# Optimization experiments

Measured on AMD Instinct MI355X. Metric: run time of the kernel, lower is better.

Reference implementation:

```python
import jax, jax.numpy as jnp
import numpy as np

B, CF, HH, WW = 32, 768, 28, 28
M, NH = 32, 1024
BETA = 0.05

def _lin(key, out_d, in_d):
    k1, k2 = jax.random.split(key)
    s = 1.0 / np.sqrt(in_d)
    W = jax.random.uniform(k1, (out_d, in_d), minval=-s, maxval=s, dtype=jnp.float32)
    b = jax.random.uniform(k2, (out_d,), minval=-s, maxval=s, dtype=jnp.float32)
    return W, b

def setup_inputs() -> dict:
    key = jax.random.key(0)
    ks = jax.random.split(key, 16)
    inp = {
        'F': jax.random.normal(ks[0], (B, CF, HH, WW), dtype=jnp.float32),
        'A': jax.random.uniform(ks[1], (B, M, HH, WW), dtype=jnp.float32),
        'C': jax.random.normal(ks[2], (1, M * CF), dtype=jnp.float32),
    }
    names = ['xi', 'hi', 'xf', 'hf', 'xo', 'ho', 'xc', 'hc']
    for i, n in enumerate(names):
        in_d = CF if n[0] == 'x' else NH
        W, b = _lin(ks[3 + i], NH, in_d)
        inp['W' + n] = W
        inp['b' + n] = b
    return inp

def reference(F, A, C, Wxi, bxi, Whi, bhi, Wxf, bxf, Whf, bhf, Wxo, bxo, Who, bho, Wxc, bxc, Whc, bhc):
    b = F.shape[0]
    hw = F.shape[2] * F.shape[3]
    m = A.shape[1]
    # BAP: avg-pool of F * A_i over spatial dims, for each attention map -> [B, M, Cf]
    V = jnp.einsum('bchw,bmhw->bmc', F, A) / hw
    V = V.reshape(b, -1)  # [B, M*Cf]
    # RCLoss (center update + detached MSE)
    tmp = jnp.sum(V - C, axis=0)  # [M*Cf]
    C_new = C + (BETA * tmp / b)[None, :]
    diff = jax.lax.stop_gradient(V) - jax.lax.stop_gradient(C_new)
    rcloss = jnp.mean(diff * diff)
    # LSTM over M steps (note: original uses sigmoid for all gates via Sig_i)
    X_seq = V.reshape(b, m, -1).transpose(1, 0, 2)  # [M, B, Cf]
    h0 = jnp.zeros((b, Whi.shape[0]), dtype=V.dtype)
    c0 = jnp.zeros((b, Whi.shape[0]), dtype=V.dtype)
    def step(carry, X):
        H, Cc = carry
        I = jax.nn.sigmoid(X @ Wxi.T + bxi + H @ Whi.T + bhi)
        Fg = jax.nn.sigmoid(X @ Wxf.T + bxf + H @ Whf.T + bhf)
        O = jax.nn.sigmoid(X @ Wxo.T + bxo + H @ Who.T + bho)
        Ct = jnp.tanh(X @ Wxc.T + bxc + H @ Whc.T + bhc)
        Cc = Fg * Cc + I * Ct
        H = O * jnp.tanh(Cc)
        return (H, Cc), None
    (H, _), _ = jax.lax.scan(step, (h0, c0), X_seq)
    return (H, rcloss, C_new)
```

## Files before the change

kernel.cpp:

```cpp
#include <hip/hip_runtime.h>
#include <math.h>

#define CF 768
#define MM 32
#define HW 784
#define MCF 24576
#define BETA 0.05f

typedef __attribute__((ext_vector_type(8))) short bf16x8;
typedef __attribute__((ext_vector_type(4))) float f32x4;

__device__ __forceinline__ float dot4(float4 a, float4 b, float acc) {
    acc = fmaf(a.x, b.x, acc); acc = fmaf(a.y, b.y, acc);
    acc = fmaf(a.z, b.z, acc); acc = fmaf(a.w, b.w, acc);
    return acc;
}

__device__ __forceinline__ unsigned short bf16rne(float x) {
    unsigned int bits = __float_as_uint(x);
    unsigned int r = (bits + 0x7fffu + ((bits >> 16) & 1u)) >> 16;
    return (unsigned short)r;
}
__device__ __forceinline__ float bf2f(unsigned short u) {
    return __uint_as_float(((unsigned int)u) << 16);
}
__device__ __forceinline__ float sigf(float x) { return 1.f / (1.f + __expf(-x)); }

#define KA_CT 96
#define KA_PAD 15

__global__ __launch_bounds__(256) void kA2(const float* __restrict__ F,
                                           const float* __restrict__ A,
                                           unsigned short* __restrict__ Vbf) {
    __shared__ float4 Fs[2][KA_CT][KA_PAD];
    __shared__ float4 As[2][32][KA_PAD];
    const int b = blockIdx.x >> 3;
    const int cbase = (blockIdx.x & 7) * KA_CT;
    const int t = threadIdx.x;
    const int tx = t & 31;
    const int ty = t >> 5;
    const int c0 = tx * 3, m0 = ty * 4;
    const float4* F4 = (const float4*)F;
    const float4* A4 = (const float4*)A;

    int i0 = t;          int fc0 = i0 / 14, fq0 = i0 - fc0 * 14;
    int i1 = t + 256;    int fc1 = i1 / 14, fq1 = i1 - fc1 * 14;
    int i2 = t + 512;    int fc2 = i2 / 14, fq2 = i2 - fc2 * 14;
    int i3 = t + 768;    int fc3 = i3 / 14, fq3 = i3 - fc3 * 14;
    int i4 = t + 1024;   int fc4 = i4 / 14, fq4 = i4 - fc4 * 14;
    int i5 = t + 1280;   int fc5 = (t < 64) ? (i5 / 14) : 0, fq5 = (t < 64) ? (i5 - (i5 / 14) * 14) : 0;
    int a0i = t;         int ac0 = a0i / 14, aq0 = a0i - ac0 * 14;
    int a1i = t + 256;   int ac1 = (t < 192) ? (a1i / 14) : 0, aq1 = (t < 192) ? (a1i - (a1i / 14) * 14) : 0;

    size_t fb0 = (size_t)(b * CF + cbase + fc0) * 196 + fq0;
    size_t fb1 = (size_t)(b * CF + cbase + fc1) * 196 + fq1;
    size_t fb2 = (size_t)(b * CF + cbase + fc2) * 196 + fq2;
    size_t fb3 = (size_t)(b * CF + cbase + fc3) * 196 + fq3;
    size_t fb4 = (size_t)(b * CF + cbase + fc4) * 196 + fq4;
    size_t fb5 = (size_t)(b * CF + cbase + fc5) * 196 + fq5;
    size_t ab0 = (size_t)(b * 32 + ac0) * 196 + aq0;
    size_t ab1 = (size_t)(b * 32 + ac1) * 196 + aq1;

    float4 fr0, fr1, fr2, fr3, fr4, fr5, ar0, ar1;
    float acc[4][3];
    #pragma unroll
    for (int i = 0; i < 4; ++i)
        #pragma unroll
        for (int j = 0; j < 3; ++j) acc[i][j] = 0.f;

    fr0 = F4[fb0]; fr1 = F4[fb1]; fr2 = F4[fb2]; fr3 = F4[fb3]; fr4 = F4[fb4];
    if (t < 64) fr5 = F4[fb5];
    ar0 = A4[ab0];
    if (t < 192) ar1 = A4[ab1];
    Fs[0][fc0][fq0] = fr0; Fs[0][fc1][fq1] = fr1; Fs[0][fc2][fq2] = fr2;
    Fs[0][fc3][fq3] = fr3; Fs[0][fc4][fq4] = fr4;
    if (t < 64) Fs[0][fc5][fq5] = fr5;
    As[0][ac0][aq0] = ar0;
    if (t < 192) As[0][ac1][aq1] = ar1;

    for (int ch = 0; ch < 14; ++ch) {
        int buf = ch & 1;
        __syncthreads();
        if (ch + 1 < 14) {
            size_t off = (size_t)(ch + 1) * 14;
            fr0 = F4[fb0 + off]; fr1 = F4[fb1 + off]; fr2 = F4[fb2 + off];
            fr3 = F4[fb3 + off]; fr4 = F4[fb4 + off];
            if (t < 64) fr5 = F4[fb5 + off];
            ar0 = A4[ab0 + off];
            if (t < 192) ar1 = A4[ab1 + off];
        }
        #pragma unroll 2
        for (int q = 0; q < 14; ++q) {
            float4 a_0 = As[buf][m0 + 0][q];
            float4 a_1 = As[buf][m0 + 1][q];
            float4 a_2 = As[buf][m0 + 2][q];
            float4 a_3 = As[buf][m0 + 3][q];
            float4 f_0 = Fs[buf][c0 + 0][q];
            float4 f_1 = Fs[buf][c0 + 1][q];
            float4 f_2 = Fs[buf][c0 + 2][q];
            acc[0][0] = dot4(a_0, f_0, acc[0][0]); acc[0][1] = dot4(a_0, f_1, acc[0][1]); acc[0][2] = dot4(a_0, f_2, acc[0][2]);
            acc[1][0] = dot4(a_1, f_0, acc[1][0]); acc[1][1] = dot4(a_1, f_1, acc[1][1]); acc[1][2] = dot4(a_1, f_2, acc[1][2]);
            acc[2][0] = dot4(a_2, f_0, acc[2][0]); acc[2][1] = dot4(a_2, f_1, acc[2][1]); acc[2][2] = dot4(a_2, f_2, acc[2][2]);
            acc[3][0] = dot4(a_3, f_0, acc[3][0]); acc[3][1] = dot4(a_3, f_1, acc[3][1]); acc[3][2] = dot4(a_3, f_2, acc[3][2]);
        }
        if (ch + 1 < 14) {
            int nb = buf ^ 1;
            Fs[nb][fc0][fq0] = fr0; Fs[nb][fc1][fq1] = fr1; Fs[nb][fc2][fq2] = fr2;
            Fs[nb][fc3][fq3] = fr3; Fs[nb][fc4][fq4] = fr4;
            if (t < 64) Fs[nb][fc5][fq5] = fr5;
            As[nb][ac0][aq0] = ar0;
            if (t < 192) As[nb][ac1][aq1] = ar1;
        }
    }
    #pragma unroll
    for (int i = 0; i < 4; ++i)
        #pragma unroll
        for (int j = 0; j < 3; ++j)
            Vbf[(size_t)(b * 32 + m0 + i) * 768 + cbase + c0 + j] =
                bf16rne(acc[i][j] * (1.f / 784.f));
}

__global__ __launch_bounds__(256) void kB1(const unsigned short* __restrict__ Vbf,
                                           const float* __restrict__ C,
                                           float* __restrict__ Cnew_out,
                                           float* __restrict__ partial) {
    int j = blockIdx.x * 256 + threadIdx.x;
    float c = C[j];
    float s = 0.f;
    for (int b = 0; b < 32; ++b) s += bf2f(Vbf[(size_t)b * MCF + j]);
    float cn = c + BETA * (s * (1.f / 32.f) - c);
    Cnew_out[j] = cn;
    float ds = 0.f;
    for (int b = 0; b < 32; ++b) {
        float d = bf2f(Vbf[(size_t)b * MCF + j]) - cn;
        ds = fmaf(d, d, ds);
    }
    __shared__ float red[256];
    red[threadIdx.x] = ds;
    __syncthreads();
    for (int off = 128; off > 0; off >>= 1) {
        if (threadIdx.x < off) red[threadIdx.x] += red[threadIdx.x + off];
        __syncthreads();
    }
    if (threadIdx.x == 0) partial[blockIdx.x] = red[0];
}

__global__ void kB2(const float* __restrict__ partial, float* __restrict__ out) {
    if (threadIdx.x == 0) {
        float s = 0.f;
        for (int i = 0; i < 96; ++i) s += partial[i];
        out[0] = s / (32.f * 24576.f);
    }
}

__global__ __launch_bounds__(256) void kPrepX(
    const float* __restrict__ Wxi, const float* __restrict__ Wxf,
    const float* __restrict__ Wxo, const float* __restrict__ Wxc,
    unsigned short* __restrict__ Wxbf) {
    int gid = blockIdx.x * 256 + threadIdx.x;
    int row = gid / 96;
    int kq = (gid - row * 96) * 8;
    int g = row >> 10, j = row & 1023;
    const float* Wg = (g == 0) ? Wxi : (g == 1) ? Wxf : (g == 2) ? Wxo : Wxc;
    const float* src = Wg + (size_t)j * CF + kq;
    float4 f0 = *(const float4*)src;
    float4 f1 = *(const float4*)(src + 4);
    unsigned short u[8];
    u[0] = bf16rne(f0.x); u[1] = bf16rne(f0.y); u[2] = bf16rne(f0.z); u[3] = bf16rne(f0.w);
    u[4] = bf16rne(f1.x); u[5] = bf16rne(f1.y); u[6] = bf16rne(f1.z); u[7] = bf16rne(f1.w);
    *(uint4*)&Wxbf[(size_t)row * CF + kq] = *(const uint4*)u;
}

__global__ __launch_bounds__(512) void kC3(
    const unsigned short* __restrict__ Vbf,
    const unsigned short* __restrict__ Wxbf,
    const float* __restrict__ bxi, const float* __restrict__ bxf,
    const float* __restrict__ bxo, const float* __restrict__ bxc,
    const float* __restrict__ bhi, const float* __restrict__ bhf,
    const float* __restrict__ bho, const float* __restrict__ bhc,
    unsigned short* __restrict__ Xbf) {
    __shared__ unsigned short Asg[512 * 8];
    const int bx = blockIdx.x;
    const int by = blockIdx.y;
    const int t = threadIdx.x;
    const int lane = t & 63;
    const int w = t >> 6;
    const int n = lane & 15;
    const int q = lane >> 4;
    const int mbase = bx * 64;

    const int st_row = (w & 3) * 16 + n;
    const int st_kb  = (w >> 2) * 4 + q;
    const int st_rg  = mbase + st_row;
    const int st_vrow = (st_rg & 31) * 32 + (st_rg >> 5);
    const unsigned short* st_src = Vbf + (size_t)st_vrow * CF + st_kb * 8;

    const int nb = by * 128 + w * 16;
    const unsigned short* Brow = Wxbf + (size_t)(nb + n) * CF + q * 8;

    f32x4 acc[4];
    #pragma unroll
    for (int g = 0; g < 4; ++g) acc[g] = (f32x4){0.f, 0.f, 0.f, 0.f};

    uint4 st = *(const uint4*)st_src;
    for (int kc = 0; kc < 12; ++kc) {
        __syncthreads();
        *(uint4*)&Asg[t * 8] = st;
        __syncthreads();
        if (kc + 1 < 12) st = *(const uint4*)(st_src + (kc + 1) * 64);
        #pragma unroll
        for (int p = 0; p < 2; ++p) {
            bf16x8 bfr = *(const bf16x8*)(Brow + kc * 64 + p * 32);
            #pragma unroll
            for (int g = 0; g < 4; ++g) {
                bf16x8 a = *(const bf16x8*)&Asg[((p * 4 + g) * 64 + lane) * 8];
                acc[g] = __builtin_amdgcn_mfma_f32_16x16x32_bf16(a, bfr, acc[g], 0, 0, 0);
            }
        }
    }

    const int gg = by >> 3;
    const int j = (by & 7) * 128 + w * 16 + n;
    const float* bx_ = (gg == 0) ? bxi : (gg == 1) ? bxf : (gg == 2) ? bxo : bxc;
    const float* bh_ = (gg == 0) ? bhi : (gg == 1) ? bhf : (gg == 2) ? bho : bhc;
    const float bias = bx_[j] + bh_[j];
    #pragma unroll
    for (int g = 0; g < 4; ++g) {
        #pragma unroll
        for (int rr = 0; rr < 4; ++rr) {
            int rg = mbase + g * 16 + q * 4 + rr;
            int tt = rg >> 5, bb = rg & 31;
            Xbf[((size_t)(tt * 4 + gg) * 32 + bb) * 1024 + j] = bf16rne(acc[g][rr] + bias);
        }
    }
}

__global__ __launch_bounds__(256) void kPrep(
    const float* __restrict__ Whi, const float* __restrict__ Whf,
    const float* __restrict__ Who, const float* __restrict__ Whc,
    unsigned short* __restrict__ Wbf) {
    size_t tid8 = ((size_t)blockIdx.x * 256 + threadIdx.x) * 8;
    int row = (int)(tid8 >> 10);
    int k = (int)(tid8 & 1023);
    int g = row >> 10, j = row & 1023;
    const float* Wg = (g == 0) ? Whi : (g == 1) ? Whf : (g == 2) ? Who : Whc;
    const float* src = Wg + (size_t)j * 1024 + k;
    float4 f0 = *(const float4*)src;
    float4 f1 = *(const float4*)(src + 4);
    unsigned short u[8];
    u[0] = bf16rne(f0.x); u[1] = bf16rne(f0.y); u[2] = bf16rne(f0.z); u[3] = bf16rne(f0.w);
    u[4] = bf16rne(f1.x); u[5] = bf16rne(f1.y); u[6] = bf16rne(f1.z); u[7] = bf16rne(f1.w);
    *(uint4*)&Wbf[tid8] = *(const uint4*)u;
}

__global__ __launch_bounds__(512) void kStep(
    const unsigned short* __restrict__ Wbf,
    const unsigned short* __restrict__ Xbf,
    const unsigned short* __restrict__ Hprev,
    unsigned short* __restrict__ Hnext,
    float* __restrict__ Cst,
    float* __restrict__ outH,
    int step) {
    __shared__ float pbuf[8][32][17];
    __shared__ float sbuf[32][17];
    const int bi = blockIdx.x;
    const int jbase = bi * 4;
    const int t = threadIdx.x;
    const int lane = t & 63;
    const int w = t >> 6;
    const int n = lane & 15;
    const int q = lane >> 4;

    if (step > 0) {
        const int g = n >> 2, jj = n & 3;
        const unsigned short* Wrow = Wbf + ((size_t)(g * 1024 + jbase + jj)) * 1024 + w * 128;
        const unsigned short* hb0 = Hprev + (size_t)n * 1024 + w * 128;
        const unsigned short* hb1 = Hprev + (size_t)(n + 16) * 1024 + w * 128;
        f32x4 acc0 = {0.f, 0.f, 0.f, 0.f};
        f32x4 acc1 = {0.f, 0.f, 0.f, 0.f};
        #pragma unroll
        for (int ks = 0; ks < 4; ++ks) {
            int k = ks * 32 + q * 8;
            bf16x8 bfrag = *(const bf16x8*)(Wrow + k);
            bf16x8 a0 = *(const bf16x8*)(hb0 + k);
            bf16x8 a1 = *(const bf16x8*)(hb1 + k);
            acc0 = __builtin_amdgcn_mfma_f32_16x16x32_bf16(a0, bfrag, acc0, 0, 0, 0);
            acc1 = __builtin_amdgcn_mfma_f32_16x16x32_bf16(a1, bfrag, acc1, 0, 0, 0);
        }
        #pragma unroll
        for (int r = 0; r < 4; ++r) {
            pbuf[w][q * 4 + r][n] = acc0[r];
            pbuf[w][16 + q * 4 + r][n] = acc1[r];
        }
    }
    __syncthreads();
    {
        int b = t >> 4, nn = t & 15;
        int g = nn >> 2, jj = nn & 3;
        float s = bf2f(Xbf[(((size_t)step * 4 + g) * 32 + b) * 1024 + jbase + jj]);
        if (step > 0) {
            #pragma unroll
            for (int w2 = 0; w2 < 8; ++w2) s += pbuf[w2][b][nn];
        }
        sbuf[b][nn] = s;
    }
    __syncthreads();
    if (t < 128) {
        int b = t >> 2, jj = t & 3;
        float I  = sigf(sbuf[b][jj]);
        float Fg = sigf(sbuf[b][4 + jj]);
        float O  = sigf(sbuf[b][8 + jj]);
        float Ct = tanhf(sbuf[b][12 + jj]);
        float cprev = (step > 0) ? Cst[b * 1024 + jbase + jj] : 0.f;
        float c = fmaf(Fg, cprev, I * Ct);
        Cst[b * 1024 + jbase + jj] = c;
        float h = O * tanhf(c);
        if (step < 31) {
            Hnext[b * 1024 + jbase + jj] = bf16rne(h);
        } else {
            outH[b * 1024 + jbase + jj] = h;
        }
    }
}

extern "C" void kernel_launch(void* const* d_in, const int* in_sizes, int n_in,
                              void* d_out, int out_size, void* d_ws, size_t ws_size,
                              hipStream_t stream) {
    const float* F   = (const float*)d_in[0];
    const float* A   = (const float*)d_in[1];
    const float* C   = (const float*)d_in[2];
    const float* Wxi = (const float*)d_in[3];
    const float* bxi = (const float*)d_in[4];
    const float* Whi = (const float*)d_in[5];
    const float* bhi = (const float*)d_in[6];
    const float* Wxf = (const float*)d_in[7];
    const float* bxf = (const float*)d_in[8];
    const float* Whf = (const float*)d_in[9];
    const float* bhf = (const float*)d_in[10];
    const float* Wxo = (const float*)d_in[11];
    const float* bxo = (const float*)d_in[12];
    const float* Who = (const float*)d_in[13];
    const float* bho = (const float*)d_in[14];
    const float* Wxc = (const float*)d_in[15];
    const float* bxc = (const float*)d_in[16];
    const float* Whc = (const float*)d_in[17];
    const float* bhc = (const float*)d_in[18];

    float* out   = (float*)d_out;
    float* outH  = out;
    float* outRC = out + 32768;
    float* outC  = out + 32769;

    float* ws = (float*)d_ws;
    unsigned short* Xbf  = (unsigned short*)ws;
    unsigned short* Wxbf = (unsigned short*)(ws + 2097152);
    unsigned short* Wbf  = (unsigned short*)(ws + 2097152);
    unsigned short* Vbf  = (unsigned short*)(ws + 4194304);
    float* part = ws + 4587520;
    unsigned short* Hbf = (unsigned short*)(ws + 4587616);
    float* Cst  = ws + 4620384;

    kA2<<<dim3(256), 256, 0, stream>>>(F, A, Vbf);
    kB1<<<dim3(96), 256, 0, stream>>>(Vbf, C, outC, part);
    kB2<<<1, 64, 0, stream>>>(part, outRC);
    kPrepX<<<dim3(1536), 256, 0, stream>>>(Wxi, Wxf, Wxo, Wxc, Wxbf);
    kC3<<<dim3(16, 32), 512, 0, stream>>>(Vbf, Wxbf,
                                          bxi, bxf, bxo, bxc,
                                          bhi, bhf, bho, bhc, Xbf);
    kPrep<<<dim3(2048), 256, 0, stream>>>(Whi, Whf, Who, Whc, Wbf);

    for (int step = 0; step < 32; ++step) {
        const unsigned short* Hprev = Hbf + ((step + 1) & 1) * 32768;
        unsigned short* Hnext = (unsigned short*)(Hbf + (step & 1) * 32768);
        kStep<<<dim3(256), 512, 0, stream>>>(Wbf, Xbf, Hprev, Hnext, Cst, outH, step);
    }
}
```

Baseline: 265.0 us.

## Use bf16 MFMA for pooling GEMM and merge prep kernels into fewer launches

Result: faster. 228.3 us (-13.9%).

```diff
diff --git a/kernel.cpp b/kernel.cpp
--- a/kernel.cpp
+++ b/kernel.cpp
@@ -10,12 +10,6 @@
 typedef __attribute__((ext_vector_type(8))) short bf16x8;
 typedef __attribute__((ext_vector_type(4))) float f32x4;
 
-__device__ __forceinline__ float dot4(float4 a, float4 b, float acc) {
-    acc = fmaf(a.x, b.x, acc); acc = fmaf(a.y, b.y, acc);
-    acc = fmaf(a.z, b.z, acc); acc = fmaf(a.w, b.w, acc);
-    return acc;
-}
-
 __device__ __forceinline__ unsigned short bf16rne(float x) {
     unsigned int bits = __float_as_uint(x);
     unsigned int r = (bits + 0x7fffu + ((bits >> 16) & 1u)) >> 16;
@@ -25,150 +19,191 @@
     return __uint_as_float(((unsigned int)u) << 16);
 }
 __device__ __forceinline__ float sigf(float x) { return 1.f / (1.f + __expf(-x)); }
-
-#define KA_CT 96
-#define KA_PAD 15
-
-__global__ __launch_bounds__(256) void kA2(const float* __restrict__ F,
-                                           const float* __restrict__ A,
+__device__ __forceinline__ float ftanh(float x) {
+    x = fminf(fmaxf(x, -12.f), 12.f);
+    float e = __expf(2.f * x);
+    return (e - 1.f) / (e + 1.f);
+}
+
+__device__ __forceinline__ void cvt8(const float4 a, const float4 b, unsigned short* u) {
+    u[0] = bf16rne(a.x); u[1] = bf16rne(a.y); u[2] = bf16rne(a.z); u[3] = bf16rne(a.w);
+    u[4] = bf16rne(b.x); u[5] = bf16rne(b.y); u[6] = bf16rne(b.z); u[7] = bf16rne(b.w);
+}
+
+__global__ __launch_bounds__(256) void kA3(const float* __restrict__ F,
+                                           const float* __restrict__ Ain,
                                            unsigned short* __restrict__ Vbf) {
-    __shared__ float4 Fs[2][KA_CT][KA_PAD];
-    __shared__ float4 As[2][32][KA_PAD];
-    const int b = blockIdx.x >> 3;
-    const int cbase = (blockIdx.x & 7) * KA_CT;
+    __shared__ unsigned short Alds[3328 * 8];
+    __shared__ unsigned short Flds[2][512 * 8];
+    const int bid = blockIdx.x;
+    const int b = bid / 12, ct = bid - b * 12;
+    const int cbase = ct * 64;
     const int t = threadIdx.x;
-    const int tx = t & 31;
-    const int ty = t >> 5;
-    const int c0 = tx * 3, m0 = ty * 4;
-    const float4* F4 = (const float4*)F;
-    const float4* A4 = (const float4*)A;
-
-    int i0 = t;          int fc0 = i0 / 14, fq0 = i0 - fc0 * 14;
-    int i1 = t + 256;    int fc1 = i1 / 14, fq1 = i1 - fc1 * 14;
-    int i2 = t + 512;    int fc2 = i2 / 14, fq2 = i2 - fc2 * 14;
-    int i3 = t + 768;    int fc3 = i3 / 14, fq3 = i3 - fc3 * 14;
-    int i4 = t + 1024;   int fc4 = i4 / 14, fq4 = i4 - fc4 * 14;
-    int i5 = t + 1280;   int fc5 = (t < 64) ? (i5 / 14) : 0, fq5 = (t < 64) ? (i5 - (i5 / 14) * 14) : 0;
-    int a0i = t;         int ac0 = a0i / 14, aq0 = a0i - ac0 * 14;
-    int a1i = t + 256;   int ac1 = (t < 192) ? (a1i / 14) : 0, aq1 = (t < 192) ? (a1i - (a1i / 14) * 14) : 0;
-
-    size_t fb0 = (size_t)(b * CF + cbase + fc0) * 196 + fq0;
-    size_t fb1 = (size_t)(b * CF + cbase + fc1) * 196 + fq1;
-    size_t fb2 = (size_t)(b * CF + cbase + fc2) * 196 + fq2;
-    size_t fb3 = (size_t)(b * CF + cbase + fc3) * 196 + fq3;
-    size_t fb4 = (size_t)(b * CF + cbase + fc4) * 196 + fq4;
-    size_t fb5 = (size_t)(b * CF + cbase + fc5) * 196 + fq5;
-    size_t ab0 = (size_t)(b * 32 + ac0) * 196 + aq0;
-    size_t ab1 = (size_t)(b * 32 + ac1) * 196 + aq1;
-
-    float4 fr0, fr1, fr2, fr3, fr4, fr5, ar0, ar1;
-    float acc[4][3];
+    const int lane = t & 63, w = t >> 6;
+    const int n = lane & 15, q = lane >> 4;
+
+    {
+        float4 va[7][2];
+        #pragma unroll
+        for (int it = 0; it < 7; ++it) {
+            int s = it * 256 + t;
+            int lf = s & 63, mk = s >> 6;
+            int m = (mk & 1) * 16 + (lf & 15);
+            int k = (mk >> 1) * 32 + (lf >> 4) * 8;
+            if (k < 784) {
+                const float* src = Ain + ((size_t)(b * 32 + m)) * 784 + k;
+                va[it][0] = *(const float4*)src;
+                va[it][1] = *(const float4*)(src + 4);
+            } else {
+                va[it][0] = (float4){0, 0, 0, 0};
+                va[it][1] = (float4){0, 0, 0, 0};
+            }
+        }
+        #pragma unroll
+        for (int it = 0; it < 7; ++it) {
+            int s = it * 256 + t;
+            unsigned short u[8];
+            cvt8(va[it][0], va[it][1], u);
+            *(uint4*)&Alds[s * 8] = *(const uint4*)u;
+        }
+        float4 vb[6][2];
+        #pragma unroll
+        for (int it = 0; it < 6; ++it) {
+            int s = (it + 7) * 256 + t;
+            int lf = s & 63, mk = s >> 6;
+            int m = (mk & 1) * 16 + (lf & 15);
+            int k = (mk >> 1) * 32 + (lf >> 4) * 8;
+            if (k < 784) {
+                const float* src = Ain + ((size_t)(b * 32 + m)) * 784 + k;
+                vb[it][0] = *(const float4*)src;
+                vb[it][1] = *(const float4*)(src + 4);
+            } else {
+                vb[it][0] = (float4){0, 0, 0, 0};
+                vb[it][1] = (float4){0, 0, 0, 0};
+            }
+        }
+        #pragma unroll
+        for (int it = 0; it < 6; ++it) {
+            int s = (it + 7) * 256 + t;
+            unsigned short u[8];
+            cvt8(vb[it][0], vb[it][1], u);
+            *(uint4*)&Alds[s * 8] = *(const uint4*)u;
+        }
+    }
+
+    float4 pf[2][2];
+    const int s0 = t, s1 = t + 256;
+    const int ls0 = s0 & 63, kc20 = (s0 >> 6) & 1, nt0 = s0 >> 7;
+    const int ls1 = s1 & 63, kc21 = (s1 >> 6) & 1, nt1 = s1 >> 7;
+    const int fc0 = nt0 * 16 + (ls0 & 15), fk0 = kc20 * 32 + (ls0 >> 4) * 8;
+    const int fc1 = nt1 * 16 + (ls1 & 15), fk1 = kc21 * 32 + (ls1 >> 4) * 8;
+    const float* Fr0 = F + ((size_t)(b * 768) + cbase + fc0) * 784;
+    const float* Fr1 = F + ((size_t)(b * 768) + cbase + fc1) * 784;
+    pf[0][0] = *(const float4*)(Fr0 + fk0); pf[0][1] = *(const float4*)(Fr0 + fk0 + 4);
+    pf[1][0] = *(const float4*)(Fr1 + fk1); pf[1][1] = *(const float4*)(Fr1 + fk1 + 4);
+    {
+        unsigned short u[8];
+        cvt8(pf[0][0], pf[0][1], u); *(uint4*)&Flds[0][s0 * 8] = *(const uint4*)u;
+        cvt8(pf[1][0], pf[1][1], u); *(uint4*)&Flds[0][s1 * 8] = *(const uint4*)u;
+    }
+    __syncthreads();
+
+    f32x4 acc[2];
+    acc[0] = (f32x4){0, 0, 0, 0};
+    acc[1] = (f32x4){0, 0, 0, 0};
+
+    for (int c13 = 0; c13 < 13; ++c13) {
+        const int buf = c13 & 1;
+        if (c13 < 12) {
+            int k0 = (c13 + 1) * 64 + fk0;
+            int k1 = (c13 + 1) * 64 + fk1;
+            if (k0 < 784) {
+                pf[0][0] = *(const float4*)(Fr0 + k0); pf[0][1] = *(const float4*)(Fr0 + k0 + 4);
+            } else { pf[0][0] = (float4){0,0,0,0}; pf[0][1] = (float4){0,0,0,0}; }
+            if (k1 < 784) {
+                pf[1][0] = *(const float4*)(Fr1 + k1); pf[1][1] = *(const float4*)(Fr1 + k1 + 4);
+            } else { pf[1][0] = (float4){0,0,0,0}; pf[1][1] = (float4){0,0,0,0}; }
+        }
+        #pragma unroll
+        for (int kc2 = 0; kc2 < 2; ++kc2) {
+            const int kc = c13 * 2 + kc2;
+            bf16x8 bfr = *(const bf16x8*)&Flds[buf][((w * 2 + kc2) * 64 + lane) * 8];
+            bf16x8 a0 = *(const bf16x8*)&Alds[((kc * 2 + 0) * 64 + lane) * 8];
+            bf16x8 a1 = *(const bf16x8*)&Alds[((kc * 2 + 1) * 64 + lane) * 8];
+            acc[0] = __builtin_amdgcn_mfma_f32_16x16x32_bf16(a0, bfr, acc[0], 0, 0, 0);
+            acc[1] = __builtin_amdgcn_mfma_f32_16x16x32_bf16(a1, bfr, acc[1], 0, 0, 0);
+        }
+        if (c13 < 12) {
+            unsigned short u[8];
+            cvt8(pf[0][0], pf[0][1], u); *(uint4*)&Flds[buf ^ 1][s0 * 8] = *(const uint4*)u;
+            cvt8(pf[1][0], pf[1][1], u); *(uint4*)&Flds[buf ^ 1][s1 * 8] = *(const uint4*)u;
+        }
+        __syncthreads();
+    }
+
     #pragma unroll
-    for (int i = 0; i < 4; ++i)
-        #pragma unroll
-        for (int j = 0; j < 3; ++j) acc[i][j] = 0.f;
-
-    fr0 = F4[fb0]; fr1 = F4[fb1]; fr2 = F4[fb2]; fr3 = F4[fb3]; fr4 = F4[fb4];
-    if (t < 64) fr5 = F4[fb5];
-    ar0 = A4[ab0];
-    if (t < 192) ar1 = A4[ab1];
-    Fs[0][fc0][fq0] = fr0; Fs[0][fc1][fq1] = fr1; Fs[0][fc2][fq2] = fr2;
-    Fs[0][fc3][fq3] = fr3; Fs[0][fc4][fq4] = fr4;
-    if (t < 64) Fs[0][fc5][fq5] = fr5;
-    As[0][ac0][aq0] = ar0;
-    if (t < 192) As[0][ac1][aq1] = ar1;
-
-    for (int ch = 0; ch < 14; ++ch) {
-        int buf = ch & 1;
-        __syncthreads();
-        if (ch + 1 < 14) {
-            size_t off = (size_t)(ch + 1) * 14;
-            fr0 = F4[fb0 + off]; fr1 = F4[fb1 + off]; fr2 = F4[fb2 + off];
-            fr3 = F4[fb3 + off]; fr4 = F4[fb4 + off];
-            if (t < 64) fr5 = F4[fb5 + off];
-            ar0 = A4[ab0 + off];
-            if (t < 192) ar1 = A4[ab1 + off];
-        }
-        #pragma unroll 2
-        for (int q = 0; q < 14; ++q) {
-            float4 a_0 = As[buf][m0 + 0][q];
-            float4 a_1 = As[buf][m0 + 1][q];
-            float4 a_2 = As[buf][m0 + 2][q];
-            float4 a_3 = As[buf][m0 + 3][q];
-            float4 f_0 = Fs[buf][c0 + 0][q];
-            float4 f_1 = Fs[buf][c0 + 1][q];
-            float4 f_2 = Fs[buf][c0 + 2][q];
-            acc[0][0] = dot4(a_0, f_0, acc[0][0]); acc[0][1] = dot4(a_0, f_1, acc[0][1]); acc[0][2] = dot4(a_0, f_2, acc[0][2]);
-            acc[1][0] = dot4(a_1, f_0, acc[1][0]); acc[1][1] = dot4(a_1, f_1, acc[1][1]); acc[1][2] = dot4(a_1, f_2, acc[1][2]);
-            acc[2][0] = dot4(a_2, f_0, acc[2][0]); acc[2][1] = dot4(a_2, f_1, acc[2][1]); acc[2][2] = dot4(a_2, f_2, acc[2][2]);
-            acc[3][0] = dot4(a_3, f_0, acc[3][0]); acc[3][1] = dot4(a_3, f_1, acc[3][1]); acc[3][2] = dot4(a_3, f_2, acc[3][2]);
-        }
-        if (ch + 1 < 14) {
-            int nb = buf ^ 1;
-            Fs[nb][fc0][fq0] = fr0; Fs[nb][fc1][fq1] = fr1; Fs[nb][fc2][fq2] = fr2;
-            Fs[nb][fc3][fq3] = fr3; Fs[nb][fc4][fq4] = fr4;
-            if (t < 64) Fs[nb][fc5][fq5] = fr5;
-            As[nb][ac0][aq0] = ar0;
-            if (t < 192) As[nb][ac1][aq1] = ar1;
-        }
-    }
-    #pragma unroll
-    for (int i = 0; i < 4; ++i)
-        #pragma unroll
-        for (int j = 0; j < 3; ++j)
-            Vbf[(size_t)(b * 32 + m0 + i) * 768 + cbase + c0 + j] =
-                bf16rne(acc[i][j] * (1.f / 784.f));
-}
-
-__global__ __launch_bounds__(256) void kB1(const unsigned short* __restrict__ Vbf,
-                                           const float* __restrict__ C,
-                                           float* __restrict__ Cnew_out,
-                                           float* __restrict__ partial) {
-    int j = blockIdx.x * 256 + threadIdx.x;
-    float c = C[j];
-    float s = 0.f;
-    for (int b = 0; b < 32; ++b) s += bf2f(Vbf[(size_t)b * MCF + j]);
-    float cn = c + BETA * (s * (1.f / 32.f) - c);
-    Cnew_out[j] = cn;
-    float ds = 0.f;
-    for (int b = 0; b < 32; ++b) {
-        float d = bf2f(Vbf[(size_t)b * MCF + j]) - cn;
-        ds = fmaf(d, d, ds);
-    }
-    __shared__ float red[256];
-    red[threadIdx.x] = ds;
-    __syncthreads();
-    for (int off = 128; off > 0; off >>= 1) {
-        if (threadIdx.x < off) red[threadIdx.x] += red[threadIdx.x + off];
-        __syncthreads();
-    }
-    if (threadIdx.x == 0) partial[blockIdx.x] = red[0];
-}
-
-__global__ void kB2(const float* __restrict__ partial, float* __restrict__ out) {
-    if (threadIdx.x == 0) {
-        float s = 0.f;
-        for (int i = 0; i < 96; ++i) s += partial[i];
-        out[0] = s / (32.f * 24576.f);
-    }
-}
-
-__global__ __launch_bounds__(256) void kPrepX(
+    for (int mt = 0; mt < 2; ++mt)
+        #pragma unroll
+        for (int r = 0; r < 4; ++r)
+            Vbf[(size_t)(b * 32 + mt * 16 + q * 4 + r) * 768 + cbase + w * 16 + n] =
+                bf16rne(acc[mt][r] * (1.f / 784.f));
+}
+
+__global__ __launch_bounds__(256) void kMisc(
+    const unsigned short* __restrict__ Vbf, const float* __restrict__ C,
+    float* __restrict__ Cnew_out, float* __restrict__ partial,
     const float* __restrict__ Wxi, const float* __restrict__ Wxf,
     const float* __restrict__ Wxo, const float* __restrict__ Wxc,
-    unsigned short* __restrict__ Wxbf) {
-    int gid = blockIdx.x * 256 + threadIdx.x;
-    int row = gid / 96;
-    int kq = (gid - row * 96) * 8;
-    int g = row >> 10, j = row & 1023;
-    const float* Wg = (g == 0) ? Wxi : (g == 1) ? Wxf : (g == 2) ? Wxo : Wxc;
-    const float* src = Wg + (size_t)j * CF + kq;
-    float4 f0 = *(const float4*)src;
-    float4 f1 = *(const float4*)(src + 4);
-    unsigned short u[8];
-    u[0] = bf16rne(f0.x); u[1] = bf16rne(f0.y); u[2] = bf16rne(f0.z); u[3] = bf16rne(f0.w);
-    u[4] = bf16rne(f1.x); u[5] = bf16rne(f1.y); u[6] = bf16rne(f1.z); u[7] = bf16rne(f1.w);
-    *(uint4*)&Wxbf[(size_t)row * CF + kq] = *(const uint4*)u;
+    unsigned short* __restrict__ Wxbf,
+    const float* __restrict__ Whi, const float* __restrict__ Whf,
+    const float* __restrict__ Who, const float* __restrict__ Whc,
+    unsigned short* __restrict__ Wbf) {
+    const int bid = blockIdx.x;
+    if (bid < 96) {
+        int j = bid * 256 + threadIdx.x;
+        float c = C[j];
+        float s = 0.f;
+        for (int b = 0; b < 32; ++b) s += bf2f(Vbf[(size_t)b * MCF + j]);
+        float cn = c + BETA * (s * (1.f / 32.f) - c);
+        Cnew_out[j] = cn;
+        float ds = 0.f;
+        for (int b = 0; b < 32; ++b) {
+            float d = bf2f(Vbf[(size_t)b * MCF + j]) - cn;
+            ds = fmaf(d, d, ds);
+        }
+        __shared__ float red[256];
+        red[threadIdx.x] = ds;
+        __syncthreads();
+        for (int off = 128; off > 0; off >>= 1) {
+            if (threadIdx.x < off) red[threadIdx.x] += red[threadIdx.x + off];
+            __syncthreads();
+        }
+        if (threadIdx.x == 0) partial[bid] = red[0];
+    } else if (bid < 1632) {
+        int gid = (bid - 96) * 256 + threadIdx.x;
+        int row = gid / 96;
+        int kq = (gid - row * 96) * 8;
+        int g = row >> 10, j = row & 1023;
+        const float* Wg = (g == 0) ? Wxi : (g == 1) ? Wxf : (g == 2) ? Wxo : Wxc;
+        const float* src = Wg + (size_t)j * CF + kq;
+        float4 f0 = *(const float4*)src;
+        float4 f1 = *(const float4*)(src + 4);
+        unsigned short u[8];
+        cvt8(f0, f1, u);
+        *(uint4*)&Wxbf[(size_t)row * CF + kq] = *(const uint4*)u;
+    } else {
+        size_t tid8 = ((size_t)(bid - 1632) * 256 + threadIdx.x) * 8;
+        int row = (int)(tid8 >> 10);
+        int k = (int)(tid8 & 1023);
+        int g = row >> 10, j = row & 1023;
+        const float* Wg = (g == 0) ? Whi : (g == 1) ? Whf : (g == 2) ? Who : Whc;
+        const float* src = Wg + (size_t)j * 1024 + k;
+        float4 f0 = *(const float4*)src;
+        float4 f1 = *(const float4*)(src + 4);
+        unsigned short u[8];
+        cvt8(f0, f1, u);
+        *(uint4*)&Wbf[tid8] = *(const uint4*)u;
+    }
 }
 
 __global__ __launch_bounds__(512) void kC3(
@@ -178,7 +213,8 @@
     const float* __restrict__ bxo, const float* __restrict__ bxc,
     const float* __restrict__ bhi, const float* __restrict__ bhf,
     const float* __restrict__ bho, const float* __restrict__ bhc,
-    unsigned short* __restrict__ Xbf) {
+    unsigned short* __restrict__ Xbf,
+    const float* __restrict__ partial, float* __restrict__ outRC) {
     __shared__ unsigned short Asg[512 * 8];
     const int bx = blockIdx.x;
     const int by = blockIdx.y;
@@ -233,24 +269,19 @@
             Xbf[((size_t)(tt * 4 + gg) * 32 + bb) * 1024 + j] = bf16rne(acc[g][rr] + bias);
         }
     }
-}
-
-__global__ __launch_bounds__(256) void kPrep(
-    const float* __restrict__ Whi, const float* __restrict__ Whf,
-    const float* __restrict__ Who, const float* __restrict__ Whc,
-    unsigned short* __restrict__ Wbf) {
-    size_t tid8 = ((size_t)blockIdx.x * 256 + threadIdx.x) * 8;
-    int row = (int)(tid8 >> 10);
-    int k = (int)(tid8 & 1023);
-    int g = row >> 10, j = row & 1023;
-    const float* Wg = (g == 0) ? Whi : (g == 1) ? Whf : (g == 2) ? Who : Whc;
-    const float* src = Wg + (size_t)j * 1024 + k;
-    float4 f0 = *(const float4*)src;
-    float4 f1 = *(const float4*)(src + 4);
-    unsigned short u[8];
-    u[0] = bf16rne(f0.x); u[1] = bf16rne(f0.y); u[2] = bf16rne(f0.z); u[3] = bf16rne(f0.w);
-    u[4] = bf16rne(f1.x); u[5] = bf16rne(f1.y); u[6] = bf16rne(f1.z); u[7] = bf16rne(f1.w);
-    *(uint4*)&Wbf[tid8] = *(const uint4*)u;
+
+    if (bx == 0 && by == 31) {
+        __syncthreads();
+        float* red = (float*)Asg;
+        float v = (t < 96) ? partial[t] : 0.f;
+        red[t] = v;
+        __syncthreads();
+        for (int off = 256; off > 0; off >>= 1) {
+            if (t < off) red[t] += red[t + off];
+            __syncthreads();
+        }
+        if (t == 0) outRC[0] = red[0] / (32.f * 24576.f);
+    }
 }
 
 __global__ __launch_bounds__(512) void kStep(
@@ -271,6 +302,12 @@
     const int n = lane & 15;
     const int q = lane >> 4;
 
+    const int pb = t >> 4, pnn = t & 15;
+    const int pg = pnn >> 2, pjj = pnn & 3;
+    const float xv = bf2f(Xbf[(((size_t)step * 4 + pg) * 32 + pb) * 1024 + jbase + pjj]);
+    float cprev = 0.f;
+    if (step > 0 && t < 128) cprev = Cst[(t >> 2) * 1024 + jbase + (t & 3)];
+
     if (step > 0) {
         const int g = n >> 2, jj = n & 3;
         const unsigned short* Wrow = Wbf + ((size_t)(g * 1024 + jbase + jj)) * 1024 + w * 128;
@@ -295,14 +332,12 @@
     }
     __syncthreads();
     {
-        int b = t >> 4, nn = t & 15;
-        int g = nn >> 2, jj = nn & 3;
-        float s = bf2f(Xbf[(((size_t)step * 4 + g) * 32 + b) * 1024 + jbase + jj]);
+        float s = xv;
         if (step > 0) {
             #pragma unroll
-            for (int w2 = 0; w2 < 8; ++w2) s += pbuf[w2][b][nn];
-        }
-        sbuf[b][nn] = s;
+            for (int w2 = 0; w2 < 8; ++w2) s += pbuf[w2][pb][pnn];
+        }
+        sbuf[pb][pnn] = s;
     }
     __syncthreads();
     if (t < 128) {
@@ -310,11 +345,10 @@
         float I  = sigf(sbuf[b][jj]);
         float Fg = sigf(sbuf[b][4 + jj]);
         float O  = sigf(sbuf[b][8 + jj]);
-        float Ct = tanhf(sbuf[b][12 + jj]);
-        float cprev = (step > 0) ? Cst[b * 1024 + jbase + jj] : 0.f;
+        float Ct = ftanh(sbuf[b][12 + jj]);
         float c = fmaf(Fg, cprev, I * Ct);
         Cst[b * 1024 + jbase + jj] = c;
-        float h = O * tanhf(c);
+        float h = O * ftanh(c);
         if (step < 31) {
             Hnext[b * 1024 + jbase + jj] = bf16rne(h);
         } else {
@@ -354,20 +388,20 @@
     float* ws = (float*)d_ws;
     unsigned short* Xbf  = (unsigned short*)ws;
     unsigned short* Wxbf = (unsigned short*)(ws + 2097152);
-    unsigned short* Wbf  = (unsigned short*)(ws + 2097152);
-    unsigned short* Vbf  = (unsigned short*)(ws + 4194304);
-    float* part = ws + 4587520;
-    unsigned short* Hbf = (unsigned short*)(ws + 4587616);
-    float* Cst  = ws + 4620384;
-
-    kA2<<<dim3(256), 256, 0, stream>>>(F, A, Vbf);
-    kB1<<<dim3(96), 256, 0, stream>>>(Vbf, C, outC, part);
-    kB2<<<1, 64, 0, stream>>>(part, outRC);
-    kPrepX<<<dim3(1536), 256, 0, stream>>>(Wxi, Wxf, Wxo, Wxc, Wxbf);
+    unsigned short* Wbf  = (unsigned short*)(ws + 3670016);
+    unsigned short* Vbf  = (unsigned short*)(ws + 5767168);
+    float* part = ws + 6160384;
+    unsigned short* Hbf = (unsigned short*)(ws + 6160480);
+    float* Cst  = ws + 6193248;
+
+    kA3<<<dim3(384), 256, 0, stream>>>(F, A, Vbf);
+    kMisc<<<dim3(3680), 256, 0, stream>>>(Vbf, C, outC, part,
+                                          Wxi, Wxf, Wxo, Wxc, Wxbf,
+                                          Whi, Whf, Who, Whc, Wbf);
     kC3<<<dim3(16, 32), 512, 0, stream>>>(Vbf, Wxbf,
                                           bxi, bxf, bxo, bxc,
-                                          bhi, bhf, bho, bhc, Xbf);
-    kPrep<<<dim3(2048), 256, 0, stream>>>(Whi, Whf, Who, Whc, Wbf);
+                                          bhi, bhf, bho, bhc, Xbf,
+                                          part, outRC);
 
     for (int step = 0; step < 32; ++step) {
         const unsigned short* Hprev = Hbf + ((step + 1) & 1) * 32768;
```
